# Kernel optimization log

Hardware: AMD Instinct MI355X
Metric: run time of the kernel (lower is better)

The kernel has to match this reference:

```python
import jax, jax.numpy as jnp
import numpy as np

INPUT_SIZE = 784
HIDDEN_SIZE = 256
NUM_CLASSES = 10
BATCH = 32768


def setup_inputs() -> dict:
    key = jax.random.key(0)
    k_x, k_w1, k_b1, k_w2, k_b2 = jax.random.split(key, 5)
    return {
        "x": jax.random.normal(k_x, (BATCH, INPUT_SIZE), dtype=jnp.float32),
        "fc1_weight": jax.random.normal(k_w1, (HIDDEN_SIZE, INPUT_SIZE), dtype=jnp.float32),
        "fc1_bias": jax.random.normal(k_b1, (HIDDEN_SIZE,), dtype=jnp.float32),
        "fc2_weight": jax.random.normal(k_w2, (NUM_CLASSES, HIDDEN_SIZE), dtype=jnp.float32),
        "fc2_bias": jax.random.normal(k_b2, (NUM_CLASSES,), dtype=jnp.float32),
    }


def reference(x, fc1_weight, fc1_bias, fc2_weight, fc2_bias):
    # hidden = x @ W1^T + b1, ReLU
    hidden = jnp.einsum("bi,hi->bh", x, fc1_weight) + fc1_bias
    activated = jnp.maximum(hidden, 0.0)
    # output = activated @ W2^T + b2
    logits = jnp.einsum("bh,ch->bc", activated, fc2_weight) + fc2_bias
    return jax.nn.softmax(logits, axis=-1)
```

## Files before the change

kernel.cpp:

```cpp
#include <hip/hip_runtime.h>
#include <math.h>

#define BATCH_N   32768
#define IN_F      784
#define HID_F     256
#define NCLS      10
#define BM        128
#define NTHREADS  512

typedef __attribute__((ext_vector_type(8)))  short short8;
typedef __attribute__((ext_vector_type(4)))  float f32x4;
typedef __attribute__((ext_vector_type(16))) float f32x16;

#define WS_W1H 0
#define WS_W1L 401408

union S8U { short8 s; uint4 u; };

__device__ __forceinline__ void cvt8(float4 a, float4 b, short8* hi, short8* lo) {
    const unsigned M = 0xFFFF0000u;
    const unsigned ux = __float_as_uint(a.x), uy = __float_as_uint(a.y),
                   uz = __float_as_uint(a.z), uw = __float_as_uint(a.w),
                   vx = __float_as_uint(b.x), vy = __float_as_uint(b.y),
                   vz = __float_as_uint(b.z), vw = __float_as_uint(b.w);
    S8U h, l;
    h.u.x = (ux >> 16) | (uy & M);
    h.u.y = (uz >> 16) | (uw & M);
    h.u.z = (vx >> 16) | (vy & M);
    h.u.w = (vz >> 16) | (vw & M);
    const float rx = a.x - __uint_as_float(ux & M);
    const float ry = a.y - __uint_as_float(uy & M);
    const float rz = a.z - __uint_as_float(uz & M);
    const float rw = a.w - __uint_as_float(uw & M);
    const float sx = b.x - __uint_as_float(vx & M);
    const float sy = b.y - __uint_as_float(vy & M);
    const float sz = b.z - __uint_as_float(vz & M);
    const float sw_ = b.w - __uint_as_float(vw & M);
    l.u.x = (__float_as_uint(rx) >> 16) | (__float_as_uint(ry) & M);
    l.u.y = (__float_as_uint(rz) >> 16) | (__float_as_uint(rw) & M);
    l.u.z = (__float_as_uint(sx) >> 16) | (__float_as_uint(sy) & M);
    l.u.w = (__float_as_uint(sz) >> 16) | (__float_as_uint(sw_) & M);
    *hi = h.s; *lo = l.s;
}

__device__ __forceinline__ void cvt8v(f32x4 a, f32x4 b, short8* hi, short8* lo) {
    float4 fa = make_float4(a[0], a[1], a[2], a[3]);
    float4 fb = make_float4(b[0], b[1], b[2], b[3]);
    cvt8(fa, fb, hi, lo);
}

__global__ __launch_bounds__(256)
void prep_w1_kernel(const float* __restrict__ w1, char* __restrict__ ws) {
    const int s    = blockIdx.x * 256 + threadIdx.x;
    const int lane = s & 63, ct = (s >> 6) & 7, kt = s >> 9;
    const int n    = ct * 32 + (lane & 31);
    const int k0   = kt * 16 + (lane >> 5) * 8;
    const float* p = w1 + (size_t)n * IN_F + k0;
    const float4 a = *(const float4*)p;
    const float4 b = *(const float4*)(p + 4);
    short8 hi, lo;
    cvt8(a, b, &hi, &lo);
    *(short8*)(ws + WS_W1H + (size_t)s * 16) = hi;
    *(short8*)(ws + WS_W1L + (size_t)s * 16) = lo;
}

__device__ __forceinline__ short8 gload_s8(const void* p) {
    short8 r;
    asm volatile("global_load_dwordx4 %0, %1, off" : "=v"(r) : "v"(p));
    return r;
}
__device__ __forceinline__ f32x4 gload_f4(const float* p) {
    f32x4 r;
    asm volatile("global_load_dwordx4 %0, %1, off" : "=v"(r) : "v"(p));
    return r;
}

#define MFMA32(A, B, C) __builtin_amdgcn_mfma_f32_32x32x16_bf16((A), (B), (C), 0, 0, 0)

#define MFMA_KT(BUF, KTL, BH, BL)                                              \
    {                                                                          \
        __builtin_amdgcn_s_setprio(1);                                         \
        _Pragma("unroll")                                                      \
        for (int rt = 0; rt < 4; ++rt) {                                       \
            const short8 ah = *(const short8*)((BUF) + (KTL) * 4096 + rt * 1024 + aro); \
            const short8 al = *(const short8*)((BUF) + 16384 + (KTL) * 4096 + rt * 1024 + aro); \
            acc[rt] = MFMA32(ah, BH, acc[rt]);                                 \
            acc[rt] = MFMA32(al, BH, acc[rt]);                                 \
            acc[rt] = MFMA32(ah, BL, acc[rt]);                                 \
        }                                                                      \
        __builtin_amdgcn_s_setprio(0);                                         \
    }

#define XISSUE4(G) do {                                                        \
        s0 = gload_f4(xs + ((G) + 1) * 64 + sq * 8);                           \
        s1 = gload_f4(xs + ((G) + 1) * 64 + sq * 8 + 4);                       \
        s2 = gload_f4(xs + ((G) + 1) * 64 + 32 + sq * 8);                      \
        s3 = gload_f4(xs + ((G) + 1) * 64 + 32 + sq * 8 + 4);                  \
    } while (0)
#define XISSUET() do {                                                         \
        s0 = gload_f4(xs + 768 + (sq & 1) * 8);                                \
        s1 = gload_f4(xs + 768 + (sq & 1) * 8 + 4);                            \
    } while (0)
#define CVT4W(BW) do {                                                         \
        short8 h0, l0, h1, l1;                                                 \
        cvt8v(s0, s1, &h0, &l0);                                               \
        cvt8v(s2, s3, &h1, &l1);                                               \
        *(short8*)((BW) + wo0)         = h0;                                   \
        *(short8*)((BW) + 16384 + wo0) = l0;                                   \
        *(short8*)((BW) + wo1)         = h1;                                   \
        *(short8*)((BW) + 16384 + wo1) = l1;                                   \
    } while (0)
#define CVTTW(BW) do {                                                         \
        short8 h0, l0;                                                         \
        cvt8v(s0, s1, &h0, &l0);                                               \
        if (sq < 2) {                                                          \
            *(short8*)((BW) + wot)         = h0;                               \
            *(short8*)((BW) + 16384 + wot) = l0;                               \
        }                                                                      \
    } while (0)

#define ROUND(G, W1, XI, CVTW)                                                 \
    {                                                                          \
        const char* bufr = sm.stage[(G) & 1];                                  \
        char* bufw = sm.stage[((G) + 1) & 1];                                  \
        bhO = gload_s8(bhp + (size_t)(4 * (G) + 1) * 8192);                    \
        blO = gload_s8(blp + (size_t)(4 * (G) + 1) * 8192);                    \
        asm volatile("s_waitcnt vmcnt(2)" ::: "memory");                       \
        __builtin_amdgcn_sched_barrier(0);                                     \
        MFMA_KT(bufr, 0, bhE, blE);                                            \
        bhE = gload_s8(bhp + (size_t)(4 * (G) + 2) * 8192);                    \
        blE = gload_s8(blp + (size_t)(4 * (G) + 2) * 8192);                    \
        XI;                                                                    \
        asm volatile(W1 ::: "memory");                                         \
        __builtin_amdgcn_sched_barrier(0);                                     \
        MFMA_KT(bufr, 1, bhO, blO);                                            \
        bhO = gload_s8(bhp + (size_t)(4 * (G) + 3) * 8192);                    \
        blO = gload_s8(blp + (size_t)(4 * (G) + 3) * 8192);                    \
        asm volatile(W1 ::: "memory");                                         \
        __builtin_amdgcn_sched_barrier(0);                                     \
        MFMA_KT(bufr, 2, bhE, blE);                                            \
        bhE = gload_s8(bhp + (size_t)(4 * (G) + 4) * 8192);                    \
        blE = gload_s8(blp + (size_t)(4 * (G) + 4) * 8192);                    \
        asm volatile("s_waitcnt vmcnt(2)" ::: "memory");                       \
        __builtin_amdgcn_sched_barrier(0);                                     \
        MFMA_KT(bufr, 3, bhO, blO);                                            \
        CVTW(bufw);                                                            \
        asm volatile("s_waitcnt lgkmcnt(0)" ::: "memory");                     \
        __builtin_amdgcn_sched_barrier(0);                                     \
        __builtin_amdgcn_s_barrier();                                          \
        __builtin_amdgcn_sched_barrier(0);                                     \
    }

__global__ __launch_bounds__(NTHREADS, 2)
void mlp_mfma_kernel(const float* __restrict__ x,
                     const char*  __restrict__ wsb,
                     const float* __restrict__ b1,
                     const float* __restrict__ w2,
                     const float* __restrict__ b2,
                     float* __restrict__ out)
{
    __shared__ union {
        char  stage[2][32768];
        float hid[64 * 256];
    } sm;

    const int tid   = threadIdx.x;
    const int lane  = tid & 63;
    const int wv    = tid >> 6;
    const int l31   = lane & 31;
    const int khalf = lane >> 5;
    const int row0  = blockIdx.x * BM;

    const int sr  = tid >> 2;
    const int sq  = tid & 3;
    const float* xs = x + (size_t)(row0 + sr) * IN_F;
    const int ssw = (sr >> 2) & 1;
    const int wo0 = (sq >> 1) * 4096 + sr * 32 + (((sq & 1) ^ ssw) << 4);
    const int wo1 = wo0 + 8192;
    const int wot = sr * 32 + ((sq ^ ssw) << 4);

    const int asw = (l31 >> 2) & 1;
    const int aro = l31 * 32 + ((khalf ^ asw) << 4);

    const char* bhp = wsb + WS_W1H + ((size_t)wv * 64 + lane) * 16;
    const char* blp = wsb + WS_W1L + ((size_t)wv * 64 + lane) * 16;

    f32x16 acc[4];
    #pragma unroll
    for (int rt = 0; rt < 4; ++rt)
        #pragma unroll
        for (int r = 0; r < 16; ++r) acc[rt][r] = 0.f;

    short8 bhE, blE, bhO, blO;
    f32x4 s0, s1, s2, s3;

    s0 = gload_f4(xs + sq * 8);
    s1 = gload_f4(xs + sq * 8 + 4);
    s2 = gload_f4(xs + 32 + sq * 8);
    s3 = gload_f4(xs + 32 + sq * 8 + 4);
    bhE = gload_s8(bhp);
    blE = gload_s8(blp);
    asm volatile("s_waitcnt vmcnt(2)" ::: "memory");
    __builtin_amdgcn_sched_barrier(0);
    CVT4W(sm.stage[0]);
    asm volatile("s_waitcnt lgkmcnt(0)" ::: "memory");
    __builtin_amdgcn_sched_barrier(0);
    __builtin_amdgcn_s_barrier();
    __builtin_amdgcn_sched_barrier(0);

    ROUND(0,  "s_waitcnt vmcnt(6)", XISSUE4(0),  CVT4W)
    ROUND(1,  "s_waitcnt vmcnt(6)", XISSUE4(1),  CVT4W)
    ROUND(2,  "s_waitcnt vmcnt(6)", XISSUE4(2),  CVT4W)
    ROUND(3,  "s_waitcnt vmcnt(6)", XISSUE4(3),  CVT4W)
    ROUND(4,  "s_waitcnt vmcnt(6)", XISSUE4(4),  CVT4W)
    ROUND(5,  "s_waitcnt vmcnt(6)", XISSUE4(5),  CVT4W)
    ROUND(6,  "s_waitcnt vmcnt(6)", XISSUE4(6),  CVT4W)
    ROUND(7,  "s_waitcnt vmcnt(6)", XISSUE4(7),  CVT4W)
    ROUND(8,  "s_waitcnt vmcnt(6)", XISSUE4(8),  CVT4W)
    ROUND(9,  "s_waitcnt vmcnt(6)", XISSUE4(9),  CVT4W)
    ROUND(10, "s_waitcnt vmcnt(6)", XISSUE4(10), CVT4W)
    ROUND(11, "s_waitcnt vmcnt(4)", XISSUET(),   CVTTW)
    {
        asm volatile("s_waitcnt vmcnt(0)" ::: "memory");
        __builtin_amdgcn_sched_barrier(0);
        MFMA_KT(sm.stage[0], 0, bhE, blE);
    }

    const int rl    = tid >> 3;
    const int slice = tid & 7;
    const int sw2   = (rl & 7) << 2;

    #pragma unroll
    for (int half = 0; half < 2; ++half) {
        __syncthreads();
        {
            const int col = wv * 32 + l31;
            const float bv = b1[col];
            #pragma unroll
            for (int rr = 0; rr < 2; ++rr) {
                const int rt = half * 2 + rr;
                #pragma unroll
                for (int reg = 0; reg < 16; ++reg) {
                    const int row = rr * 32 + (reg & 3) + 8 * (reg >> 2) + 4 * khalf;
                    sm.hid[row * 256 + (col ^ ((row & 7) << 2))] =
                        fmaxf(acc[rt][reg] + bv, 0.f);
                }
            }
        }
        __syncthreads();
        float lg[NCLS];
        #pragma unroll
        for (int k = 0; k < NCLS; ++k) lg[k] = 0.f;
        #pragma unroll
        for (int i = 0; i < 8; ++i) {
            const int ii  = ((i + slice) & 7) * 4;
            const int col = slice * 32 + ii;
            const float4 h = *(const float4*)(sm.hid + rl * 256 + (slice * 32 + (ii ^ sw2)));
            #pragma unroll
            for (int k = 0; k < NCLS; ++k) {
                const float4 w = *(const float4*)(w2 + k * HID_F + col);
                lg[k] += h.x * w.x + h.y * w.y + h.z * w.z + h.w * w.w;
            }
        }
        #pragma unroll
        for (int k = 0; k < NCLS; ++k) {
            float v = lg[k];
            v += __shfl_xor(v, 1);
            v += __shfl_xor(v, 2);
            v += __shfl_xor(v, 4);
            lg[k] = v + b2[k];
        }
        float mx = -1e30f;
        #pragma unroll
        for (int k = 0; k < NCLS; ++k) mx = fmaxf(mx, lg[k]);
        float s = 0.f;
        #pragma unroll
        for (int k = 0; k < NCLS; ++k) { lg[k] = __expf(lg[k] - mx); s += lg[k]; }
        const float inv = 1.f / s;
        const float va = (slice & 4)
            ? ((slice & 2) ? ((slice & 1) ? lg[7] : lg[6]) : ((slice & 1) ? lg[5] : lg[4]))
            : ((slice & 2) ? ((slice & 1) ? lg[3] : lg[2]) : ((slice & 1) ? lg[1] : lg[0]));
        const float vb = (slice & 1) ? lg[9] : lg[8];
        float* o = out + (size_t)(row0 + half * 64 + rl) * NCLS;
        o[slice] = va * inv;
        if (slice < 2) o[8 + slice] = vb * inv;
    }
}

extern "C" void kernel_launch(void* const* d_in, const int* in_sizes, int n_in,
                              void* d_out, int out_size, void* d_ws, size_t ws_size,
                              hipStream_t stream)
{
    const float* x  = (const float*)d_in[0];
    const float* w1 = (const float*)d_in[1];
    const float* b1 = (const float*)d_in[2];
    const float* w2 = (const float*)d_in[3];
    const float* b2 = (const float*)d_in[4];
    float* out = (float*)d_out;

    hipLaunchKernelGGL(prep_w1_kernel, dim3(98), dim3(256), 0, stream,
                       w1, (char*)d_ws);
    hipLaunchKernelGGL(mlp_mfma_kernel, dim3(BATCH_N / BM), dim3(NTHREADS), 0, stream,
                       x, (const char*)d_ws, b1, w2, b2, out);
}
```

Measured before the change: 187.7 us.

## Double threads per block and split row tiles across wave groups

```diff
diff --git a/kernel.cpp b/kernel.cpp
--- a/kernel.cpp
+++ b/kernel.cpp
@@ -6,7 +6,7 @@
 #define HID_F     256
 #define NCLS      10
 #define BM        128
-#define NTHREADS  512
+#define NTHREADS  1024
 
 typedef __attribute__((ext_vector_type(8)))  short short8;
 typedef __attribute__((ext_vector_type(4)))  float f32x4;
@@ -77,49 +77,46 @@
 
 #define MFMA32(A, B, C) __builtin_amdgcn_mfma_f32_32x32x16_bf16((A), (B), (C), 0, 0, 0)
 
-#define MFMA_KT(BUF, KTL, BH, BL)                                              \
+#define MFMA_KT(BUF, T, BH, BL)                                                \
     {                                                                          \
+        const short8 ah0 = *(const short8*)((BUF) + rb0 + (((T) ^ txor) << 5));\
+        const short8 al0 = *(const short8*)((BUF) + 16384 + rb0 + (((T) ^ txor) << 5)); \
+        const short8 ah1 = *(const short8*)((BUF) + rb1 + (((T) ^ txor) << 5));\
+        const short8 al1 = *(const short8*)((BUF) + 16384 + rb1 + (((T) ^ txor) << 5)); \
         __builtin_amdgcn_s_setprio(1);                                         \
-        _Pragma("unroll")                                                      \
-        for (int rt = 0; rt < 4; ++rt) {                                       \
-            const short8 ah = *(const short8*)((BUF) + (KTL) * 4096 + rt * 1024 + aro); \
-            const short8 al = *(const short8*)((BUF) + 16384 + (KTL) * 4096 + rt * 1024 + aro); \
-            acc[rt] = MFMA32(ah, BH, acc[rt]);                                 \
-            acc[rt] = MFMA32(al, BH, acc[rt]);                                 \
-            acc[rt] = MFMA32(ah, BL, acc[rt]);                                 \
-        }                                                                      \
+        acc0 = MFMA32(ah0, BH, acc0);                                          \
+        acc0 = MFMA32(al0, BH, acc0);                                          \
+        acc0 = MFMA32(ah0, BL, acc0);                                          \
+        acc1 = MFMA32(ah1, BH, acc1);                                          \
+        acc1 = MFMA32(al1, BH, acc1);                                          \
+        acc1 = MFMA32(ah1, BL, acc1);                                          \
         __builtin_amdgcn_s_setprio(0);                                         \
     }
 
-#define XISSUE4(G) do {                                                        \
-        s0 = gload_f4(xs + ((G) + 1) * 64 + sq * 8);                           \
-        s1 = gload_f4(xs + ((G) + 1) * 64 + sq * 8 + 4);                       \
-        s2 = gload_f4(xs + ((G) + 1) * 64 + 32 + sq * 8);                      \
-        s3 = gload_f4(xs + ((G) + 1) * 64 + 32 + sq * 8 + 4);                  \
+#define XISSUE(G) do {                                                         \
+        s0 = gload_f4(xs + ((G) + 1) * 64 + sc * 8);                           \
+        s1 = gload_f4(xs + ((G) + 1) * 64 + sc * 8 + 4);                       \
     } while (0)
 #define XISSUET() do {                                                         \
-        s0 = gload_f4(xs + 768 + (sq & 1) * 8);                                \
-        s1 = gload_f4(xs + 768 + (sq & 1) * 8 + 4);                            \
+        s0 = gload_f4(xs + 768 + shf * 8);                                     \
+        s1 = gload_f4(xs + 768 + shf * 8 + 4);                                 \
     } while (0)
 #define CVT4W(BW) do {                                                         \
-        short8 h0, l0, h1, l1;                                                 \
+        short8 h0, l0;                                                         \
         cvt8v(s0, s1, &h0, &l0);                                               \
-        cvt8v(s2, s3, &h1, &l1);                                               \
-        *(short8*)((BW) + wo0)         = h0;                                   \
-        *(short8*)((BW) + 16384 + wo0) = l0;                                   \
-        *(short8*)((BW) + wo1)         = h1;                                   \
-        *(short8*)((BW) + 16384 + wo1) = l1;                                   \
+        *(short8*)((BW) + wo)         = h0;                                    \
+        *(short8*)((BW) + 16384 + wo) = l0;                                    \
     } while (0)
 #define CVTTW(BW) do {                                                         \
         short8 h0, l0;                                                         \
         cvt8v(s0, s1, &h0, &l0);                                               \
-        if (sq < 2) {                                                          \
+        if (sc < 2) {                                                          \
             *(short8*)((BW) + wot)         = h0;                               \
             *(short8*)((BW) + 16384 + wot) = l0;                               \
         }                                                                      \
     } while (0)
 
-#define ROUND(G, W1, XI, CVTW)                                                 \
+#define ROUND(G, XI, CVTW)                                                     \
     {                                                                          \
         const char* bufr = sm.stage[(G) & 1];                                  \
         char* bufw = sm.stage[((G) + 1) & 1];                                  \
@@ -131,12 +128,12 @@
         bhE = gload_s8(bhp + (size_t)(4 * (G) + 2) * 8192);                    \
         blE = gload_s8(blp + (size_t)(4 * (G) + 2) * 8192);                    \
         XI;                                                                    \
-        asm volatile(W1 ::: "memory");                                         \
+        asm volatile("s_waitcnt vmcnt(4)" ::: "memory");                       \
         __builtin_amdgcn_sched_barrier(0);                                     \
         MFMA_KT(bufr, 1, bhO, blO);                                            \
         bhO = gload_s8(bhp + (size_t)(4 * (G) + 3) * 8192);                    \
         blO = gload_s8(blp + (size_t)(4 * (G) + 3) * 8192);                    \
-        asm volatile(W1 ::: "memory");                                         \
+        asm volatile("s_waitcnt vmcnt(4)" ::: "memory");                       \
         __builtin_amdgcn_sched_barrier(0);                                     \
         MFMA_KT(bufr, 2, bhE, blE);                                            \
         bhE = gload_s8(bhp + (size_t)(4 * (G) + 4) * 8192);                    \
@@ -151,7 +148,7 @@
         __builtin_amdgcn_sched_barrier(0);                                     \
     }
 
-__global__ __launch_bounds__(NTHREADS, 2)
+__global__ __launch_bounds__(NTHREADS, 4)
 void mlp_mfma_kernel(const float* __restrict__ x,
                      const char*  __restrict__ wsb,
                      const float* __restrict__ b1,
@@ -167,37 +164,37 @@
     const int tid   = threadIdx.x;
     const int lane  = tid & 63;
     const int wv    = tid >> 6;
+    const int ct    = wv & 7;
+    const int rg    = wv >> 3;
     const int l31   = lane & 31;
     const int khalf = lane >> 5;
     const int row0  = blockIdx.x * BM;
 
-    const int sr  = tid >> 2;
-    const int sq  = tid & 3;
+    const int sr  = tid >> 3;
+    const int sc  = tid & 7;
+    const int shf = sc & 1;
     const float* xs = x + (size_t)(row0 + sr) * IN_F;
     const int ssw = (sr >> 2) & 1;
-    const int wo0 = (sq >> 1) * 4096 + sr * 32 + (((sq & 1) ^ ssw) << 4);
-    const int wo1 = wo0 + 8192;
-    const int wot = sr * 32 + ((sq ^ ssw) << 4);
-
-    const int asw = (l31 >> 2) & 1;
-    const int aro = l31 * 32 + ((khalf ^ asw) << 4);
-
-    const char* bhp = wsb + WS_W1H + ((size_t)wv * 64 + lane) * 16;
-    const char* blp = wsb + WS_W1L + ((size_t)wv * 64 + lane) * 16;
-
-    f32x16 acc[4];
+    const int wo  = sr * 128 + (((sc >> 1) ^ (sr & 3)) & 3) * 32 + ((shf ^ ssw) << 4);
+    const int wot = sr * 128 + ((sr & 3) << 5) + ((shf ^ ssw) << 4);
+
+    const int txor = l31 & 3;
+    const int asw  = (l31 >> 2) & 1;
+    const int rb0  = (rg * 64 + l31) * 128 + ((khalf ^ asw) << 4);
+    const int rb1  = rb0 + 4096;
+
+    const char* bhp = wsb + WS_W1H + ((size_t)ct * 64 + lane) * 16;
+    const char* blp = wsb + WS_W1L + ((size_t)ct * 64 + lane) * 16;
+
+    f32x16 acc0, acc1;
     #pragma unroll
-    for (int rt = 0; rt < 4; ++rt)
-        #pragma unroll
-        for (int r = 0; r < 16; ++r) acc[rt][r] = 0.f;
+    for (int r = 0; r < 16; ++r) { acc0[r] = 0.f; acc1[r] = 0.f; }
 
     short8 bhE, blE, bhO, blO;
-    f32x4 s0, s1, s2, s3;
-
-    s0 = gload_f4(xs + sq * 8);
-    s1 = gload_f4(xs + sq * 8 + 4);
-    s2 = gload_f4(xs + 32 + sq * 8);
-    s3 = gload_f4(xs + 32 + sq * 8 + 4);
+    f32x4 s0, s1;
+
+    s0 = gload_f4(xs + sc * 8);
+    s1 = gload_f4(xs + sc * 8 + 4);
     bhE = gload_s8(bhp);
     blE = gload_s8(blp);
     asm volatile("s_waitcnt vmcnt(2)" ::: "memory");
@@ -208,43 +205,43 @@
     __builtin_amdgcn_s_barrier();
     __builtin_amdgcn_sched_barrier(0);
 
-    ROUND(0,  "s_waitcnt vmcnt(6)", XISSUE4(0),  CVT4W)
-    ROUND(1,  "s_waitcnt vmcnt(6)", XISSUE4(1),  CVT4W)
-    ROUND(2,  "s_waitcnt vmcnt(6)", XISSUE4(2),  CVT4W)
-    ROUND(3,  "s_waitcnt vmcnt(6)", XISSUE4(3),  CVT4W)
-    ROUND(4,  "s_waitcnt vmcnt(6)", XISSUE4(4),  CVT4W)
-    ROUND(5,  "s_waitcnt vmcnt(6)", XISSUE4(5),  CVT4W)
-    ROUND(6,  "s_waitcnt vmcnt(6)", XISSUE4(6),  CVT4W)
-    ROUND(7,  "s_waitcnt vmcnt(6)", XISSUE4(7),  CVT4W)
-    ROUND(8,  "s_waitcnt vmcnt(6)", XISSUE4(8),  CVT4W)
-    ROUND(9,  "s_waitcnt vmcnt(6)", XISSUE4(9),  CVT4W)
-    ROUND(10, "s_waitcnt vmcnt(6)", XISSUE4(10), CVT4W)
-    ROUND(11, "s_waitcnt vmcnt(4)", XISSUET(),   CVTTW)
+    ROUND(0,  XISSUE(0),  CVT4W)
+    ROUND(1,  XISSUE(1),  CVT4W)
+    ROUND(2,  XISSUE(2),  CVT4W)
+    ROUND(3,  XISSUE(3),  CVT4W)
+    ROUND(4,  XISSUE(4),  CVT4W)
+    ROUND(5,  XISSUE(5),  CVT4W)
+    ROUND(6,  XISSUE(6),  CVT4W)
+    ROUND(7,  XISSUE(7),  CVT4W)
+    ROUND(8,  XISSUE(8),  CVT4W)
+    ROUND(9,  XISSUE(9),  CVT4W)
+    ROUND(10, XISSUE(10), CVT4W)
+    ROUND(11, XISSUET(),  CVTTW)
     {
         asm volatile("s_waitcnt vmcnt(0)" ::: "memory");
         __builtin_amdgcn_sched_barrier(0);
         MFMA_KT(sm.stage[0], 0, bhE, blE);
     }
 
-    const int rl    = tid >> 3;
-    const int slice = tid & 7;
+    const int rl    = tid >> 4;
+    const int slice = tid & 15;
     const int sw2   = (rl & 7) << 2;
 
+    __syncthreads();
     #pragma unroll
-    for (int half = 0; half < 2; ++half) {
-        __syncthreads();
-        {
-            const int col = wv * 32 + l31;
+    for (int hf = 0; hf < 2; ++hf) {
+        if (hf) __syncthreads();
+        if (rg == hf) {
+            const int col = ct * 32 + l31;
             const float bv = b1[col];
             #pragma unroll
-            for (int rr = 0; rr < 2; ++rr) {
-                const int rt = half * 2 + rr;
-                #pragma unroll
-                for (int reg = 0; reg < 16; ++reg) {
-                    const int row = rr * 32 + (reg & 3) + 8 * (reg >> 2) + 4 * khalf;
-                    sm.hid[row * 256 + (col ^ ((row & 7) << 2))] =
-                        fmaxf(acc[rt][reg] + bv, 0.f);
-                }
+            for (int reg = 0; reg < 16; ++reg) {
+                const int crow = (reg & 3) + 8 * (reg >> 2) + 4 * khalf;
+                sm.hid[crow * 256 + (col ^ ((crow & 7) << 2))] =
+                    fmaxf(acc0[reg] + bv, 0.f);
+                const int drow = 32 + crow;
+                sm.hid[drow * 256 + (col ^ ((drow & 7) << 2))] =
+                    fmaxf(acc1[reg] + bv, 0.f);
             }
         }
         __syncthreads();
@@ -252,10 +249,10 @@
         #pragma unroll
         for (int k = 0; k < NCLS; ++k) lg[k] = 0.f;
         #pragma unroll
-        for (int i = 0; i < 8; ++i) {
-            const int ii  = ((i + slice) & 7) * 4;
-            const int col = slice * 32 + ii;
-            const float4 h = *(const float4*)(sm.hid + rl * 256 + (slice * 32 + (ii ^ sw2)));
+        for (int i = 0; i < 4; ++i) {
+            const int ii  = (i + (slice >> 1)) & 3;
+            const int col = slice * 16 + ii * 4;
+            const float4 h = *(const float4*)(sm.hid + rl * 256 + (col ^ sw2));
             #pragma unroll
             for (int k = 0; k < NCLS; ++k) {
                 const float4 w = *(const float4*)(w2 + k * HID_F + col);
@@ -268,6 +265,7 @@
             v += __shfl_xor(v, 1);
             v += __shfl_xor(v, 2);
             v += __shfl_xor(v, 4);
+            v += __shfl_xor(v, 8);
             lg[k] = v + b2[k];
         }
         float mx = -1e30f;
@@ -277,13 +275,13 @@
         #pragma unroll
         for (int k = 0; k < NCLS; ++k) { lg[k] = __expf(lg[k] - mx); s += lg[k]; }
         const float inv = 1.f / s;
-        const float va = (slice & 4)
-            ? ((slice & 2) ? ((slice & 1) ? lg[7] : lg[6]) : ((slice & 1) ? lg[5] : lg[4]))
-            : ((slice & 2) ? ((slice & 1) ? lg[3] : lg[2]) : ((slice & 1) ? lg[1] : lg[0]));
-        const float vb = (slice & 1) ? lg[9] : lg[8];
-        float* o = out + (size_t)(row0 + half * 64 + rl) * NCLS;
-        o[slice] = va * inv;
-        if (slice < 2) o[8 + slice] = vb * inv;
+        const float va = (slice & 8)
+            ? ((slice & 1) ? lg[9] : lg[8])
+            : ((slice & 4)
+                ? ((slice & 2) ? ((slice & 1) ? lg[7] : lg[6]) : ((slice & 1) ? lg[5] : lg[4]))
+                : ((slice & 2) ? ((slice & 1) ? lg[3] : lg[2]) : ((slice & 1) ? lg[1] : lg[0])));
+        if (slice < NCLS)
+            out[(size_t)(row0 + hf * 64 + rl) * NCLS + slice] = va * inv;
     }
 }
 
```

After: 195.3 us. +4.1%, slower.

## Retile fc1 MFMA warps into 2x2 row/column blocks to halve LDS A reads

Applied to the files above, without the earlier changes.

```diff
diff --git a/kernel.cpp b/kernel.cpp
--- a/kernel.cpp
+++ b/kernel.cpp
@@ -76,79 +76,91 @@
 }
 
 #define MFMA32(A, B, C) __builtin_amdgcn_mfma_f32_32x32x16_bf16((A), (B), (C), 0, 0, 0)
-
-#define MFMA_KT(BUF, KTL, BH, BL)                                              \
-    {                                                                          \
-        __builtin_amdgcn_s_setprio(1);                                         \
-        _Pragma("unroll")                                                      \
-        for (int rt = 0; rt < 4; ++rt) {                                       \
-            const short8 ah = *(const short8*)((BUF) + (KTL) * 4096 + rt * 1024 + aro); \
-            const short8 al = *(const short8*)((BUF) + 16384 + (KTL) * 4096 + rt * 1024 + aro); \
-            acc[rt] = MFMA32(ah, BH, acc[rt]);                                 \
-            acc[rt] = MFMA32(al, BH, acc[rt]);                                 \
-            acc[rt] = MFMA32(ah, BL, acc[rt]);                                 \
-        }                                                                      \
-        __builtin_amdgcn_s_setprio(0);                                         \
+#define SB __builtin_amdgcn_sched_barrier(0)
+
+#define MFMA_KT(BUF, T, S)                                                      \
+    {                                                                           \
+        const int sl = (((((T) << 1) | khalf) ^ l7) << 4);                      \
+        const short8 ah0 = *(const short8*)((BUF) + arb0 + sl);                 \
+        const short8 al0 = *(const short8*)((BUF) + 16384 + arb0 + sl);         \
+        const short8 ah1 = *(const short8*)((BUF) + arb1 + sl);                 \
+        const short8 al1 = *(const short8*)((BUF) + 16384 + arb1 + sl);         \
+        __builtin_amdgcn_s_setprio(1);                                          \
+        acc00 = MFMA32(ah0, bh0##S, acc00);                                     \
+        acc01 = MFMA32(ah0, bh1##S, acc01);                                     \
+        acc10 = MFMA32(ah1, bh0##S, acc10);                                     \
+        acc11 = MFMA32(ah1, bh1##S, acc11);                                     \
+        acc00 = MFMA32(al0, bh0##S, acc00);                                     \
+        acc01 = MFMA32(al0, bh1##S, acc01);                                     \
+        acc10 = MFMA32(al1, bh0##S, acc10);                                     \
+        acc11 = MFMA32(al1, bh1##S, acc11);                                     \
+        acc00 = MFMA32(ah0, bl0##S, acc00);                                     \
+        acc01 = MFMA32(ah0, bl1##S, acc01);                                     \
+        acc10 = MFMA32(ah1, bl0##S, acc10);                                     \
+        acc11 = MFMA32(ah1, bl1##S, acc11);                                     \
+        __builtin_amdgcn_s_setprio(0);                                          \
     }
 
-#define XISSUE4(G) do {                                                        \
-        s0 = gload_f4(xs + ((G) + 1) * 64 + sq * 8);                           \
-        s1 = gload_f4(xs + ((G) + 1) * 64 + sq * 8 + 4);                       \
-        s2 = gload_f4(xs + ((G) + 1) * 64 + 32 + sq * 8);                      \
-        s3 = gload_f4(xs + ((G) + 1) * 64 + 32 + sq * 8 + 4);                  \
+#define BISSUE(KT, S)                                                           \
+    bh0##S = gload_s8(bhp + (size_t)(KT) * 8192);                               \
+    bh1##S = gload_s8(bhp + (size_t)(KT) * 8192 + 1024);                        \
+    bl0##S = gload_s8(blp + (size_t)(KT) * 8192);                               \
+    bl1##S = gload_s8(blp + (size_t)(KT) * 8192 + 1024);
+
+#define XISSUE(G) do {                                                          \
+        s0 = gload_f4(xs + ((G) + 1) * 64 + sq * 8);                            \
+        s1 = gload_f4(xs + ((G) + 1) * 64 + sq * 8 + 4);                        \
+        s2 = gload_f4(xs + ((G) + 1) * 64 + 32 + sq * 8);                       \
+        s3 = gload_f4(xs + ((G) + 1) * 64 + 32 + sq * 8 + 4);                   \
     } while (0)
-#define XISSUET() do {                                                         \
-        s0 = gload_f4(xs + 768 + (sq & 1) * 8);                                \
-        s1 = gload_f4(xs + 768 + (sq & 1) * 8 + 4);                            \
+#define XISSUET() do {                                                          \
+        s0 = gload_f4(xs + 768 + (sq & 1) * 8);                                 \
+        s1 = gload_f4(xs + 768 + (sq & 1) * 8 + 4);                             \
     } while (0)
-#define CVT4W(BW) do {                                                         \
-        short8 h0, l0, h1, l1;                                                 \
-        cvt8v(s0, s1, &h0, &l0);                                               \
-        cvt8v(s2, s3, &h1, &l1);                                               \
-        *(short8*)((BW) + wo0)         = h0;                                   \
-        *(short8*)((BW) + 16384 + wo0) = l0;                                   \
-        *(short8*)((BW) + wo1)         = h1;                                   \
-        *(short8*)((BW) + 16384 + wo1) = l1;                                   \
+#define CVT4W(BW) do {                                                          \
+        short8 h0, l0, h1, l1;                                                  \
+        cvt8v(s0, s1, &h0, &l0);                                                \
+        cvt8v(s2, s3, &h1, &l1);                                                \
+        *(short8*)((BW) + wo0)         = h0;                                    \
+        *(short8*)((BW) + 16384 + wo0) = l0;                                    \
+        *(short8*)((BW) + wo1)         = h1;                                    \
+        *(short8*)((BW) + 16384 + wo1) = l1;                                    \
     } while (0)
-#define CVTTW(BW) do {                                                         \
-        short8 h0, l0;                                                         \
-        cvt8v(s0, s1, &h0, &l0);                                               \
-        if (sq < 2) {                                                          \
-            *(short8*)((BW) + wot)         = h0;                               \
-            *(short8*)((BW) + 16384 + wot) = l0;                               \
-        }                                                                      \
+#define CVTTW(BW) do {                                                          \
+        short8 h0, l0;                                                          \
+        cvt8v(s0, s1, &h0, &l0);                                                \
+        if (sq < 2) {                                                           \
+            *(short8*)((BW) + wo0)         = h0;                                \
+            *(short8*)((BW) + 16384 + wo0) = l0;                                \
+        }                                                                       \
     } while (0)
 
-#define ROUND(G, W1, XI, CVTW)                                                 \
-    {                                                                          \
-        const char* bufr = sm.stage[(G) & 1];                                  \
-        char* bufw = sm.stage[((G) + 1) & 1];                                  \
-        bhO = gload_s8(bhp + (size_t)(4 * (G) + 1) * 8192);                    \
-        blO = gload_s8(blp + (size_t)(4 * (G) + 1) * 8192);                    \
-        asm volatile("s_waitcnt vmcnt(2)" ::: "memory");                       \
-        __builtin_amdgcn_sched_barrier(0);                                     \
-        MFMA_KT(bufr, 0, bhE, blE);                                            \
-        bhE = gload_s8(bhp + (size_t)(4 * (G) + 2) * 8192);                    \
-        blE = gload_s8(blp + (size_t)(4 * (G) + 2) * 8192);                    \
-        XI;                                                                    \
-        asm volatile(W1 ::: "memory");                                         \
-        __builtin_amdgcn_sched_barrier(0);                                     \
-        MFMA_KT(bufr, 1, bhO, blO);                                            \
-        bhO = gload_s8(bhp + (size_t)(4 * (G) + 3) * 8192);                    \
-        blO = gload_s8(blp + (size_t)(4 * (G) + 3) * 8192);                    \
-        asm volatile(W1 ::: "memory");                                         \
-        __builtin_amdgcn_sched_barrier(0);                                     \
-        MFMA_KT(bufr, 2, bhE, blE);                                            \
-        bhE = gload_s8(bhp + (size_t)(4 * (G) + 4) * 8192);                    \
-        blE = gload_s8(blp + (size_t)(4 * (G) + 4) * 8192);                    \
-        asm volatile("s_waitcnt vmcnt(2)" ::: "memory");                       \
-        __builtin_amdgcn_sched_barrier(0);                                     \
-        MFMA_KT(bufr, 3, bhO, blO);                                            \
-        CVTW(bufw);                                                            \
-        asm volatile("s_waitcnt lgkmcnt(0)" ::: "memory");                     \
-        __builtin_amdgcn_sched_barrier(0);                                     \
-        __builtin_amdgcn_s_barrier();                                          \
-        __builtin_amdgcn_sched_barrier(0);                                     \
+#define ROUND(G, WT1, WT2, WT3, XI, CVTW)                                       \
+    {                                                                           \
+        const char* bufr = sm.stage[(G) & 1];                                   \
+        char* bufw = sm.stage[((G) + 1) & 1];                                   \
+        BISSUE(4 * (G) + 1, O)                                                  \
+        asm volatile("s_waitcnt vmcnt(4)" ::: "memory");                        \
+        SB;                                                                     \
+        MFMA_KT(bufr, 0, E)                                                     \
+        BISSUE(4 * (G) + 2, E)                                                  \
+        XI;                                                                     \
+        asm volatile(WT1 ::: "memory");                                         \
+        SB;                                                                     \
+        MFMA_KT(bufr, 1, O)                                                     \
+        BISSUE(4 * (G) + 3, O)                                                  \
+        asm volatile(WT2 ::: "memory");                                         \
+        SB;                                                                     \
+        MFMA_KT(bufr, 2, E)                                                     \
+        BISSUE(4 * (G) + 4, E)                                                  \
+        asm volatile(WT3 ::: "memory");                                         \
+        SB;                                                                     \
+        MFMA_KT(bufr, 3, O)                                                     \
+        CVTW(bufw);                                                             \
+        asm volatile("s_waitcnt lgkmcnt(0)" ::: "memory");                      \
+        SB;                                                                     \
+        __builtin_amdgcn_s_barrier();                                           \
+        SB;                                                                     \
     }
 
 __global__ __launch_bounds__(NTHREADS, 2)
@@ -167,63 +179,61 @@
     const int tid   = threadIdx.x;
     const int lane  = tid & 63;
     const int wv    = tid >> 6;
+    const int cp    = wv & 3;
+    const int rp    = wv >> 2;
     const int l31   = lane & 31;
     const int khalf = lane >> 5;
+    const int l7    = l31 & 7;
     const int row0  = blockIdx.x * BM;
 
     const int sr  = tid >> 2;
     const int sq  = tid & 3;
     const float* xs = x + (size_t)(row0 + sr) * IN_F;
-    const int ssw = (sr >> 2) & 1;
-    const int wo0 = (sq >> 1) * 4096 + sr * 32 + (((sq & 1) ^ ssw) << 4);
-    const int wo1 = wo0 + 8192;
-    const int wot = sr * 32 + ((sq ^ ssw) << 4);
-
-    const int asw = (l31 >> 2) & 1;
-    const int aro = l31 * 32 + ((khalf ^ asw) << 4);
-
-    const char* bhp = wsb + WS_W1H + ((size_t)wv * 64 + lane) * 16;
-    const char* blp = wsb + WS_W1L + ((size_t)wv * 64 + lane) * 16;
-
-    f32x16 acc[4];
+    const int wo0 = sr * 128 + ((sq ^ (sr & 7)) << 4);
+    const int wo1 = sr * 128 + (((sq + 4) ^ (sr & 7)) << 4);
+
+    const int arb0 = (rp * 64 + l31) * 128;
+    const int arb1 = arb0 + 4096;
+
+    const char* bhp = wsb + WS_W1H + ((size_t)(cp * 2) * 64 + lane) * 16;
+    const char* blp = wsb + WS_W1L + ((size_t)(cp * 2) * 64 + lane) * 16;
+
+    f32x16 acc00, acc01, acc10, acc11;
     #pragma unroll
-    for (int rt = 0; rt < 4; ++rt)
-        #pragma unroll
-        for (int r = 0; r < 16; ++r) acc[rt][r] = 0.f;
-
-    short8 bhE, blE, bhO, blO;
+    for (int r = 0; r < 16; ++r) { acc00[r] = 0.f; acc01[r] = 0.f; acc10[r] = 0.f; acc11[r] = 0.f; }
+
+    short8 bh0E, bh1E, bl0E, bl1E, bh0O, bh1O, bl0O, bl1O;
     f32x4 s0, s1, s2, s3;
 
     s0 = gload_f4(xs + sq * 8);
     s1 = gload_f4(xs + sq * 8 + 4);
     s2 = gload_f4(xs + 32 + sq * 8);
     s3 = gload_f4(xs + 32 + sq * 8 + 4);
-    bhE = gload_s8(bhp);
-    blE = gload_s8(blp);
-    asm volatile("s_waitcnt vmcnt(2)" ::: "memory");
-    __builtin_amdgcn_sched_barrier(0);
+    BISSUE(0, E)
+    asm volatile("s_waitcnt vmcnt(4)" ::: "memory");
+    SB;
     CVT4W(sm.stage[0]);
     asm volatile("s_waitcnt lgkmcnt(0)" ::: "memory");
-    __builtin_amdgcn_sched_barrier(0);
+    SB;
     __builtin_amdgcn_s_barrier();
-    __builtin_amdgcn_sched_barrier(0);
-
-    ROUND(0,  "s_waitcnt vmcnt(6)", XISSUE4(0),  CVT4W)
-    ROUND(1,  "s_waitcnt vmcnt(6)", XISSUE4(1),  CVT4W)
-    ROUND(2,  "s_waitcnt vmcnt(6)", XISSUE4(2),  CVT4W)
-    ROUND(3,  "s_waitcnt vmcnt(6)", XISSUE4(3),  CVT4W)
-    ROUND(4,  "s_waitcnt vmcnt(6)", XISSUE4(4),  CVT4W)
-    ROUND(5,  "s_waitcnt vmcnt(6)", XISSUE4(5),  CVT4W)
-    ROUND(6,  "s_waitcnt vmcnt(6)", XISSUE4(6),  CVT4W)
-    ROUND(7,  "s_waitcnt vmcnt(6)", XISSUE4(7),  CVT4W)
-    ROUND(8,  "s_waitcnt vmcnt(6)", XISSUE4(8),  CVT4W)
-    ROUND(9,  "s_waitcnt vmcnt(6)", XISSUE4(9),  CVT4W)
-    ROUND(10, "s_waitcnt vmcnt(6)", XISSUE4(10), CVT4W)
-    ROUND(11, "s_waitcnt vmcnt(4)", XISSUET(),   CVTTW)
+    SB;
+
+    ROUND(0,  "s_waitcnt vmcnt(8)", "s_waitcnt vmcnt(8)", "s_waitcnt vmcnt(4)", XISSUE(0),  CVT4W)
+    ROUND(1,  "s_waitcnt vmcnt(8)", "s_waitcnt vmcnt(8)", "s_waitcnt vmcnt(4)", XISSUE(1),  CVT4W)
+    ROUND(2,  "s_waitcnt vmcnt(8)", "s_waitcnt vmcnt(8)", "s_waitcnt vmcnt(4)", XISSUE(2),  CVT4W)
+    ROUND(3,  "s_waitcnt vmcnt(8)", "s_waitcnt vmcnt(8)", "s_waitcnt vmcnt(4)", XISSUE(3),  CVT4W)
+    ROUND(4,  "s_waitcnt vmcnt(8)", "s_waitcnt vmcnt(8)", "s_waitcnt vmcnt(4)", XISSUE(4),  CVT4W)
+    ROUND(5,  "s_waitcnt vmcnt(8)", "s_waitcnt vmcnt(8)", "s_waitcnt vmcnt(4)", XISSUE(5),  CVT4W)
+    ROUND(6,  "s_waitcnt vmcnt(8)", "s_waitcnt vmcnt(8)", "s_waitcnt vmcnt(4)", XISSUE(6),  CVT4W)
+    ROUND(7,  "s_waitcnt vmcnt(8)", "s_waitcnt vmcnt(8)", "s_waitcnt vmcnt(4)", XISSUE(7),  CVT4W)
+    ROUND(8,  "s_waitcnt vmcnt(8)", "s_waitcnt vmcnt(8)", "s_waitcnt vmcnt(4)", XISSUE(8),  CVT4W)
+    ROUND(9,  "s_waitcnt vmcnt(8)", "s_waitcnt vmcnt(8)", "s_waitcnt vmcnt(4)", XISSUE(9),  CVT4W)
+    ROUND(10, "s_waitcnt vmcnt(8)", "s_waitcnt vmcnt(8)", "s_waitcnt vmcnt(4)", XISSUE(10), CVT4W)
+    ROUND(11, "s_waitcnt vmcnt(6)", "s_waitcnt vmcnt(6)", "s_waitcnt vmcnt(4)", XISSUET(),  CVTTW)
     {
         asm volatile("s_waitcnt vmcnt(0)" ::: "memory");
-        __builtin_amdgcn_sched_barrier(0);
-        MFMA_KT(sm.stage[0], 0, bhE, blE);
+        SB;
+        MFMA_KT(sm.stage[0], 0, E)
     }
 
     const int rl    = tid >> 3;
@@ -233,17 +243,19 @@
     #pragma unroll
     for (int half = 0; half < 2; ++half) {
         __syncthreads();
-        {
-            const int col = wv * 32 + l31;
-            const float bv = b1[col];
+        if (rp == half) {
             #pragma unroll
-            for (int rr = 0; rr < 2; ++rr) {
-                const int rt = half * 2 + rr;
+            for (int c = 0; c < 2; ++c) {
+                const int col = (cp * 2 + c) * 32 + l31;
+                const float bv = b1[col];
                 #pragma unroll
                 for (int reg = 0; reg < 16; ++reg) {
-                    const int row = rr * 32 + (reg & 3) + 8 * (reg >> 2) + 4 * khalf;
-                    sm.hid[row * 256 + (col ^ ((row & 7) << 2))] =
-                        fmaxf(acc[rt][reg] + bv, 0.f);
+                    const int r0 = (reg & 3) + 8 * (reg >> 2) + 4 * khalf;
+                    const float v0 = (c == 0) ? acc00[reg] : acc01[reg];
+                    sm.hid[r0 * 256 + (col ^ ((r0 & 7) << 2))] = fmaxf(v0 + bv, 0.f);
+                    const int r1 = 32 + r0;
+                    const float v1 = (c == 0) ? acc10[reg] : acc11[reg];
+                    sm.hid[r1 * 256 + (col ^ ((r1 & 7) << 2))] = fmaxf(v1 + bv, 0.f);
                 }
             }
         }
```

Result: no change. 190.8 us (+1.7%).
